# Performance work log

Hardware: AMD Instinct MI355X
Metric: run time of the kernel (lower is better)

The kernel has to match this reference:

```python
import jax, jax.numpy as jnp
import numpy as np

B, T, D = 8, 2048, 1024
S, W = 512, 16  # num spans, span width


def setup_inputs() -> dict:
    key = jax.random.key(0)
    k1, k2, k3, k4, k5, k6, k7 = jax.random.split(key, 7)
    text_tensor = jax.random.normal(k1, (B, T, D), dtype=jnp.float32)
    contextualized_embedding = jax.random.normal(k2, (B, T, D), dtype=jnp.float32)
    word_indices = jax.random.randint(k3, (B, S, W), 0, T, dtype=jnp.int64)
    word_mask = jax.random.randint(k4, (B, S, W), 0, 2, dtype=jnp.int64)
    word_indices_mask = jax.random.randint(k5, (B, S), 0, 2, dtype=jnp.int64)
    # Linear(input_dim, 1) params
    att_w = jax.random.normal(k6, (D, 1), dtype=jnp.float32) / np.sqrt(D)
    att_b = jax.random.normal(k7, (1,), dtype=jnp.float32) * 0.01
    return {
        "text_tensor": text_tensor,
        "contextualized_embedding": contextualized_embedding,
        "word_indices": word_indices,
        "word_mask": word_mask,
        "word_indices_mask": word_indices_mask,
        "att_w": att_w,
        "att_b": att_b,
    }


def reference(text_tensor, contextualized_embedding, word_indices, word_mask,
              word_indices_mask, att_w, att_b):
    b, t, d = text_tensor.shape
    s, w = word_indices.shape[1], word_indices.shape[2]
    # per-token attention logits: [B, T]
    global_logits = (jnp.einsum("btd,do->bto", text_tensor, att_w) + att_b)[..., 0]
    # relu on indices (clamp negatives to 0), then batched gather
    idx = jnp.maximum(word_indices, 0).astype(jnp.int32)  # [B, S, W]
    flat_idx = idx.reshape(b, s * w)
    # gather span embeddings: [B, S, W, D]
    span_emb = jnp.take_along_axis(text_tensor, flat_idx[:, :, None], axis=1)
    span_emb = span_emb.reshape(b, s, w, d)
    # gather span logits: [B, S, W]
    span_logits = jnp.take_along_axis(global_logits, flat_idx, axis=1).reshape(b, s, w)
    # masked softmax over span width
    mask = word_mask.astype(jnp.bool_)
    masked_logits = jnp.where(mask, span_logits, jnp.float32(-1e9))
    weights = jax.nn.softmax(masked_logits, axis=-1) * mask.astype(span_logits.dtype)
    # weighted sum pooling: [B, S, D]
    attended = jnp.einsum("bswd,bsw->bsd", span_emb, weights)
    return attended * word_indices_mask.astype(attended.dtype)[..., None]
```

## Files before the change

kernel.cpp:

```cpp
#include <hip/hip_runtime.h>

#define NB 8
#define NT 2048
#define ND 1024
#define NS 512
#define NW 16

typedef float f32x4 __attribute__((ext_vector_type(4)));

__global__ __launch_bounds__(64) void span_attn_kernel(
    const float* __restrict__ text,
    const int*   __restrict__ wi,
    const int*   __restrict__ wm,
    const int*   __restrict__ wim,
    const float* __restrict__ att_w,
    const float* __restrict__ att_b,
    float*       __restrict__ out)
{
    const int b    = blockIdx.x & (NB - 1);
    const int s    = blockIdx.x >> 3;
    const int bs   = b * NS + s;
    const int lane = threadIdx.x;

    float* orow = out + (size_t)bs * ND + 4 * lane;

    if (wim[bs] == 0) {
        #pragma unroll
        for (int k = 0; k < 4; ++k)
            __builtin_nontemporal_store((f32x4){0.f, 0.f, 0.f, 0.f},
                reinterpret_cast<f32x4*>(orow + 256 * k));
        return;
    }

    const int* wip = wi + (size_t)bs * NW;
    const int* wmp = wm + (size_t)bs * NW;

    unsigned mkbits = 0;
    #pragma unroll
    for (int q = 0; q < 4; ++q) {
        const int4 mv = *reinterpret_cast<const int4*>(wmp + 4 * q);
        mkbits |= (mv.x != 0 ? 1u : 0u) << (4 * q + 0);
        mkbits |= (mv.y != 0 ? 1u : 0u) << (4 * q + 1);
        mkbits |= (mv.z != 0 ? 1u : 0u) << (4 * q + 2);
        mkbits |= (mv.w != 0 ? 1u : 0u) << (4 * q + 3);
    }

    f32x4 wfrag[4];
    #pragma unroll
    for (int k = 0; k < 4; ++k)
        wfrag[k] = *reinterpret_cast<const f32x4*>(att_w + 4 * lane + 256 * k);
    const float bias = att_b[0];

    const float* tbase = text + (size_t)b * NT * ND + 4 * lane;

    f32x4 acc[4];
    #pragma unroll
    for (int k = 0; k < 4; ++k) acc[k] = (f32x4){0.f, 0.f, 0.f, 0.f};
    float esum = 0.0f;

    unsigned mask = mkbits;

    while (__popc(mask) >= 4) {
        const int r0 = __builtin_ctz(mask); mask &= mask - 1;
        const int r1 = __builtin_ctz(mask); mask &= mask - 1;
        const int r2 = __builtin_ctz(mask); mask &= mask - 1;
        const int r3 = __builtin_ctz(mask); mask &= mask - 1;
        const int i0 = wip[r0], i1 = wip[r1], i2 = wip[r2], i3 = wip[r3];
        const float* s0 = tbase + (size_t)(i0 > 0 ? i0 : 0) * ND;
        const float* s1 = tbase + (size_t)(i1 > 0 ? i1 : 0) * ND;
        const float* s2 = tbase + (size_t)(i2 > 0 ? i2 : 0) * ND;
        const float* s3 = tbase + (size_t)(i3 > 0 ? i3 : 0) * ND;
        f32x4 f0[4], f1[4], f2[4], f3[4];
        #pragma unroll
        for (int k = 0; k < 4; ++k) {
            f0[k] = *reinterpret_cast<const f32x4*>(s0 + 256 * k);
            f1[k] = *reinterpret_cast<const f32x4*>(s1 + 256 * k);
            f2[k] = *reinterpret_cast<const f32x4*>(s2 + 256 * k);
            f3[k] = *reinterpret_cast<const f32x4*>(s3 + 256 * k);
        }
        float d0 = 0.f, d1 = 0.f, d2 = 0.f, d3 = 0.f;
        #pragma unroll
        for (int k = 0; k < 4; ++k) {
            d0 += f0[k].x * wfrag[k].x + f0[k].y * wfrag[k].y
                + f0[k].z * wfrag[k].z + f0[k].w * wfrag[k].w;
            d1 += f1[k].x * wfrag[k].x + f1[k].y * wfrag[k].y
                + f1[k].z * wfrag[k].z + f1[k].w * wfrag[k].w;
            d2 += f2[k].x * wfrag[k].x + f2[k].y * wfrag[k].y
                + f2[k].z * wfrag[k].z + f2[k].w * wfrag[k].w;
            d3 += f3[k].x * wfrag[k].x + f3[k].y * wfrag[k].y
                + f3[k].z * wfrag[k].z + f3[k].w * wfrag[k].w;
        }
        #pragma unroll
        for (int sh = 1; sh < 64; sh <<= 1) {
            d0 += __shfl_xor(d0, sh);
            d1 += __shfl_xor(d1, sh);
            d2 += __shfl_xor(d2, sh);
            d3 += __shfl_xor(d3, sh);
        }
        const float e0 = __expf(d0 + bias);
        const float e1 = __expf(d1 + bias);
        const float e2 = __expf(d2 + bias);
        const float e3 = __expf(d3 + bias);
        esum += (e0 + e1) + (e2 + e3);
        #pragma unroll
        for (int k = 0; k < 4; ++k) {
            acc[k].x += e0 * f0[k].x + e1 * f1[k].x + e2 * f2[k].x + e3 * f3[k].x;
            acc[k].y += e0 * f0[k].y + e1 * f1[k].y + e2 * f2[k].y + e3 * f3[k].y;
            acc[k].z += e0 * f0[k].z + e1 * f1[k].z + e2 * f2[k].z + e3 * f3[k].z;
            acc[k].w += e0 * f0[k].w + e1 * f1[k].w + e2 * f2[k].w + e3 * f3[k].w;
        }
    }

    if (__popc(mask) >= 2) {
        const int r0 = __builtin_ctz(mask); mask &= mask - 1;
        const int r1 = __builtin_ctz(mask); mask &= mask - 1;
        const int i0 = wip[r0], i1 = wip[r1];
        const float* s0 = tbase + (size_t)(i0 > 0 ? i0 : 0) * ND;
        const float* s1 = tbase + (size_t)(i1 > 0 ? i1 : 0) * ND;
        f32x4 f0[4], f1[4];
        #pragma unroll
        for (int k = 0; k < 4; ++k) {
            f0[k] = *reinterpret_cast<const f32x4*>(s0 + 256 * k);
            f1[k] = *reinterpret_cast<const f32x4*>(s1 + 256 * k);
        }
        float d0 = 0.f, d1 = 0.f;
        #pragma unroll
        for (int k = 0; k < 4; ++k) {
            d0 += f0[k].x * wfrag[k].x + f0[k].y * wfrag[k].y
                + f0[k].z * wfrag[k].z + f0[k].w * wfrag[k].w;
            d1 += f1[k].x * wfrag[k].x + f1[k].y * wfrag[k].y
                + f1[k].z * wfrag[k].z + f1[k].w * wfrag[k].w;
        }
        #pragma unroll
        for (int sh = 1; sh < 64; sh <<= 1) {
            d0 += __shfl_xor(d0, sh);
            d1 += __shfl_xor(d1, sh);
        }
        const float e0 = __expf(d0 + bias);
        const float e1 = __expf(d1 + bias);
        esum += e0 + e1;
        #pragma unroll
        for (int k = 0; k < 4; ++k) {
            acc[k].x += e0 * f0[k].x + e1 * f1[k].x;
            acc[k].y += e0 * f0[k].y + e1 * f1[k].y;
            acc[k].z += e0 * f0[k].z + e1 * f1[k].z;
            acc[k].w += e0 * f0[k].w + e1 * f1[k].w;
        }
    }

    if (mask) {
        const int r0 = __builtin_ctz(mask);
        const int i0 = wip[r0];
        const float* s0 = tbase + (size_t)(i0 > 0 ? i0 : 0) * ND;
        f32x4 f0[4];
        #pragma unroll
        for (int k = 0; k < 4; ++k)
            f0[k] = *reinterpret_cast<const f32x4*>(s0 + 256 * k);
        float d0 = 0.f;
        #pragma unroll
        for (int k = 0; k < 4; ++k)
            d0 += f0[k].x * wfrag[k].x + f0[k].y * wfrag[k].y
                + f0[k].z * wfrag[k].z + f0[k].w * wfrag[k].w;
        #pragma unroll
        for (int sh = 1; sh < 64; sh <<= 1)
            d0 += __shfl_xor(d0, sh);
        const float e0 = __expf(d0 + bias);
        esum += e0;
        #pragma unroll
        for (int k = 0; k < 4; ++k) {
            acc[k].x += e0 * f0[k].x;
            acc[k].y += e0 * f0[k].y;
            acc[k].z += e0 * f0[k].z;
            acc[k].w += e0 * f0[k].w;
        }
    }

    const float inv = esum > 0.0f ? 1.0f / esum : 0.0f;
    #pragma unroll
    for (int k = 0; k < 4; ++k) {
        f32x4 o = acc[k];
        o.x *= inv; o.y *= inv; o.z *= inv; o.w *= inv;
        __builtin_nontemporal_store(o, reinterpret_cast<f32x4*>(orow + 256 * k));
    }
}

extern "C" void kernel_launch(void* const* d_in, const int* in_sizes, int n_in,
                              void* d_out, int out_size, void* d_ws, size_t ws_size,
                              hipStream_t stream) {
    const float* text  = (const float*)d_in[0];
    const int*   wi    = (const int*)d_in[2];
    const int*   wm    = (const int*)d_in[3];
    const int*   wim   = (const int*)d_in[4];
    const float* att_w = (const float*)d_in[5];
    const float* att_b = (const float*)d_in[6];
    float*       out   = (float*)d_out;

    span_attn_kernel<<<dim3(NB * NS), dim3(64), 0, stream>>>(
        text, wi, wm, wim, att_w, att_b, out);
}
```

Measured before the change: 15.48 us.

## Use persistent blocks with atomic work-stealing over spans per batch

The launch shrinks to 2048 blocks. Each block first handles one statically assigned span, then claims further spans from a per-batch atomic counter until all 512 spans in that batch are done. The aim is to balance the uneven per-span work that comes from the random masks, and to cut block launch overhead. In exchange it adds a memset launch, one atomic per span, and a serial dependency on the counter.

Result: slower. 26.72 us (+72.6%).

```diff
diff --git a/kernel.cpp b/kernel.cpp
--- a/kernel.cpp
+++ b/kernel.cpp
@@ -15,172 +15,180 @@
     const int*   __restrict__ wim,
     const float* __restrict__ att_w,
     const float* __restrict__ att_b,
-    float*       __restrict__ out)
+    float*       __restrict__ out,
+    unsigned*    __restrict__ counters)
 {
+    const int lane = threadIdx.x;
     const int b    = blockIdx.x & (NB - 1);
-    const int s    = blockIdx.x >> 3;
-    const int bs   = b * NS + s;
-    const int lane = threadIdx.x;
-
-    float* orow = out + (size_t)bs * ND + 4 * lane;
-
-    if (wim[bs] == 0) {
-        #pragma unroll
-        for (int k = 0; k < 4; ++k)
-            __builtin_nontemporal_store((f32x4){0.f, 0.f, 0.f, 0.f},
-                reinterpret_cast<f32x4*>(orow + 256 * k));
-        return;
-    }
-
-    const int* wip = wi + (size_t)bs * NW;
-    const int* wmp = wm + (size_t)bs * NW;
-
-    unsigned mkbits = 0;
-    #pragma unroll
-    for (int q = 0; q < 4; ++q) {
-        const int4 mv = *reinterpret_cast<const int4*>(wmp + 4 * q);
-        mkbits |= (mv.x != 0 ? 1u : 0u) << (4 * q + 0);
-        mkbits |= (mv.y != 0 ? 1u : 0u) << (4 * q + 1);
-        mkbits |= (mv.z != 0 ? 1u : 0u) << (4 * q + 2);
-        mkbits |= (mv.w != 0 ? 1u : 0u) << (4 * q + 3);
-    }
+    unsigned* ctr  = counters + b * 16;
 
     f32x4 wfrag[4];
     #pragma unroll
     for (int k = 0; k < 4; ++k)
         wfrag[k] = *reinterpret_cast<const f32x4*>(att_w + 4 * lane + 256 * k);
     const float bias = att_b[0];
-
     const float* tbase = text + (size_t)b * NT * ND + 4 * lane;
 
-    f32x4 acc[4];
-    #pragma unroll
-    for (int k = 0; k < 4; ++k) acc[k] = (f32x4){0.f, 0.f, 0.f, 0.f};
-    float esum = 0.0f;
-
-    unsigned mask = mkbits;
-
-    while (__popc(mask) >= 4) {
-        const int r0 = __builtin_ctz(mask); mask &= mask - 1;
-        const int r1 = __builtin_ctz(mask); mask &= mask - 1;
-        const int r2 = __builtin_ctz(mask); mask &= mask - 1;
-        const int r3 = __builtin_ctz(mask); mask &= mask - 1;
-        const int i0 = wip[r0], i1 = wip[r1], i2 = wip[r2], i3 = wip[r3];
-        const float* s0 = tbase + (size_t)(i0 > 0 ? i0 : 0) * ND;
-        const float* s1 = tbase + (size_t)(i1 > 0 ? i1 : 0) * ND;
-        const float* s2 = tbase + (size_t)(i2 > 0 ? i2 : 0) * ND;
-        const float* s3 = tbase + (size_t)(i3 > 0 ? i3 : 0) * ND;
-        f32x4 f0[4], f1[4], f2[4], f3[4];
-        #pragma unroll
-        for (int k = 0; k < 4; ++k) {
-            f0[k] = *reinterpret_cast<const f32x4*>(s0 + 256 * k);
-            f1[k] = *reinterpret_cast<const f32x4*>(s1 + 256 * k);
-            f2[k] = *reinterpret_cast<const f32x4*>(s2 + 256 * k);
-            f3[k] = *reinterpret_cast<const f32x4*>(s3 + 256 * k);
+    int s = blockIdx.x >> 3;
+
+    while (true) {
+        const int bs = b * NS + s;
+        float* orow = out + (size_t)bs * ND + 4 * lane;
+
+        if (wim[bs] == 0) {
+            #pragma unroll
+            for (int k = 0; k < 4; ++k)
+                __builtin_nontemporal_store((f32x4){0.f, 0.f, 0.f, 0.f},
+                    reinterpret_cast<f32x4*>(orow + 256 * k));
+        } else {
+            const int* wip = wi + (size_t)bs * NW;
+            const int* wmp = wm + (size_t)bs * NW;
+
+            unsigned mask = 0;
+            #pragma unroll
+            for (int q = 0; q < 4; ++q) {
+                const int4 mv = *reinterpret_cast<const int4*>(wmp + 4 * q);
+                mask |= (mv.x != 0 ? 1u : 0u) << (4 * q + 0);
+                mask |= (mv.y != 0 ? 1u : 0u) << (4 * q + 1);
+                mask |= (mv.z != 0 ? 1u : 0u) << (4 * q + 2);
+                mask |= (mv.w != 0 ? 1u : 0u) << (4 * q + 3);
+            }
+
+            f32x4 acc[4];
+            #pragma unroll
+            for (int k = 0; k < 4; ++k) acc[k] = (f32x4){0.f, 0.f, 0.f, 0.f};
+            float esum = 0.0f;
+
+            while (__popc(mask) >= 4) {
+                const int r0 = __builtin_ctz(mask); mask &= mask - 1;
+                const int r1 = __builtin_ctz(mask); mask &= mask - 1;
+                const int r2 = __builtin_ctz(mask); mask &= mask - 1;
+                const int r3 = __builtin_ctz(mask); mask &= mask - 1;
+                const int i0 = wip[r0], i1 = wip[r1], i2 = wip[r2], i3 = wip[r3];
+                const float* s0 = tbase + (size_t)(i0 > 0 ? i0 : 0) * ND;
+                const float* s1 = tbase + (size_t)(i1 > 0 ? i1 : 0) * ND;
+                const float* s2 = tbase + (size_t)(i2 > 0 ? i2 : 0) * ND;
+                const float* s3 = tbase + (size_t)(i3 > 0 ? i3 : 0) * ND;
+                f32x4 f0[4], f1[4], f2[4], f3[4];
+                #pragma unroll
+                for (int k = 0; k < 4; ++k) {
+                    f0[k] = *reinterpret_cast<const f32x4*>(s0 + 256 * k);
+                    f1[k] = *reinterpret_cast<const f32x4*>(s1 + 256 * k);
+                    f2[k] = *reinterpret_cast<const f32x4*>(s2 + 256 * k);
+                    f3[k] = *reinterpret_cast<const f32x4*>(s3 + 256 * k);
+                }
+                float d0 = 0.f, d1 = 0.f, d2 = 0.f, d3 = 0.f;
+                #pragma unroll
+                for (int k = 0; k < 4; ++k) {
+                    d0 += f0[k].x * wfrag[k].x + f0[k].y * wfrag[k].y
+                        + f0[k].z * wfrag[k].z + f0[k].w * wfrag[k].w;
+                    d1 += f1[k].x * wfrag[k].x + f1[k].y * wfrag[k].y
+                        + f1[k].z * wfrag[k].z + f1[k].w * wfrag[k].w;
+                    d2 += f2[k].x * wfrag[k].x + f2[k].y * wfrag[k].y
+                        + f2[k].z * wfrag[k].z + f2[k].w * wfrag[k].w;
+                    d3 += f3[k].x * wfrag[k].x + f3[k].y * wfrag[k].y
+                        + f3[k].z * wfrag[k].z + f3[k].w * wfrag[k].w;
+                }
+                #pragma unroll
+                for (int sh = 1; sh < 64; sh <<= 1) {
+                    d0 += __shfl_xor(d0, sh);
+                    d1 += __shfl_xor(d1, sh);
+                    d2 += __shfl_xor(d2, sh);
+                    d3 += __shfl_xor(d3, sh);
+                }
+                const float e0 = __expf(d0 + bias);
+                const float e1 = __expf(d1 + bias);
+                const float e2 = __expf(d2 + bias);
+                const float e3 = __expf(d3 + bias);
+                esum += (e0 + e1) + (e2 + e3);
+                #pragma unroll
+                for (int k = 0; k < 4; ++k) {
+                    acc[k].x += e0 * f0[k].x + e1 * f1[k].x + e2 * f2[k].x + e3 * f3[k].x;
+                    acc[k].y += e0 * f0[k].y + e1 * f1[k].y + e2 * f2[k].y + e3 * f3[k].y;
+                    acc[k].z += e0 * f0[k].z + e1 * f1[k].z + e2 * f2[k].z + e3 * f3[k].z;
+                    acc[k].w += e0 * f0[k].w + e1 * f1[k].w + e2 * f2[k].w + e3 * f3[k].w;
+                }
+            }
+
+            if (__popc(mask) >= 2) {
+                const int r0 = __builtin_ctz(mask); mask &= mask - 1;
+                const int r1 = __builtin_ctz(mask); mask &= mask - 1;
+                const int i0 = wip[r0], i1 = wip[r1];
+                const float* s0 = tbase + (size_t)(i0 > 0 ? i0 : 0) * ND;
+                const float* s1 = tbase + (size_t)(i1 > 0 ? i1 : 0) * ND;
+                f32x4 f0[4], f1[4];
+                #pragma unroll
+                for (int k = 0; k < 4; ++k) {
+                    f0[k] = *reinterpret_cast<const f32x4*>(s0 + 256 * k);
+                    f1[k] = *reinterpret_cast<const f32x4*>(s1 + 256 * k);
+                }
+                float d0 = 0.f, d1 = 0.f;
+                #pragma unroll
+                for (int k = 0; k < 4; ++k) {
+                    d0 += f0[k].x * wfrag[k].x + f0[k].y * wfrag[k].y
+                        + f0[k].z * wfrag[k].z + f0[k].w * wfrag[k].w;
+                    d1 += f1[k].x * wfrag[k].x + f1[k].y * wfrag[k].y
+                        + f1[k].z * wfrag[k].z + f1[k].w * wfrag[k].w;
+                }
+                #pragma unroll
+                for (int sh = 1; sh < 64; sh <<= 1) {
+                    d0 += __shfl_xor(d0, sh);
+                    d1 += __shfl_xor(d1, sh);
+                }
+                const float e0 = __expf(d0 + bias);
+                const float e1 = __expf(d1 + bias);
+                esum += e0 + e1;
+                #pragma unroll
+                for (int k = 0; k < 4; ++k) {
+                    acc[k].x += e0 * f0[k].x + e1 * f1[k].x;
+                    acc[k].y += e0 * f0[k].y + e1 * f1[k].y;
+                    acc[k].z += e0 * f0[k].z + e1 * f1[k].z;
+                    acc[k].w += e0 * f0[k].w + e1 * f1[k].w;
+                }
+            }
+
+            if (mask) {
+                const int r0 = __builtin_ctz(mask);
+                const int i0 = wip[r0];
+                const float* s0 = tbase + (size_t)(i0 > 0 ? i0 : 0) * ND;
+                f32x4 f0[4];
+                #pragma unroll
+                for (int k = 0; k < 4; ++k)
+                    f0[k] = *reinterpret_cast<const f32x4*>(s0 + 256 * k);
+                float d0 = 0.f;
+                #pragma unroll
+                for (int k = 0; k < 4; ++k)
+                    d0 += f0[k].x * wfrag[k].x + f0[k].y * wfrag[k].y
+                        + f0[k].z * wfrag[k].z + f0[k].w * wfrag[k].w;
+                #pragma unroll
+                for (int sh = 1; sh < 64; sh <<= 1)
+                    d0 += __shfl_xor(d0, sh);
+                const float e0 = __expf(d0 + bias);
+                esum += e0;
+                #pragma unroll
+                for (int k = 0; k < 4; ++k) {
+                    acc[k].x += e0 * f0[k].x;
+                    acc[k].y += e0 * f0[k].y;
+                    acc[k].z += e0 * f0[k].z;
+                    acc[k].w += e0 * f0[k].w;
+                }
+            }
+
+            const float inv = esum > 0.0f ? 1.0f / esum : 0.0f;
+            #pragma unroll
+            for (int k = 0; k < 4; ++k) {
+                f32x4 o = acc[k];
+                o.x *= inv; o.y *= inv; o.z *= inv; o.w *= inv;
+                __builtin_nontemporal_store(o,
+                    reinterpret_cast<f32x4*>(orow + 256 * k));
+            }
         }
-        float d0 = 0.f, d1 = 0.f, d2 = 0.f, d3 = 0.f;
-        #pragma unroll
-        for (int k = 0; k < 4; ++k) {
-            d0 += f0[k].x * wfrag[k].x + f0[k].y * wfrag[k].y
-                + f0[k].z * wfrag[k].z + f0[k].w * wfrag[k].w;
-            d1 += f1[k].x * wfrag[k].x + f1[k].y * wfrag[k].y
-                + f1[k].z * wfrag[k].z + f1[k].w * wfrag[k].w;
-            d2 += f2[k].x * wfrag[k].x + f2[k].y * wfrag[k].y
-                + f2[k].z * wfrag[k].z + f2[k].w * wfrag[k].w;
-            d3 += f3[k].x * wfrag[k].x + f3[k].y * wfrag[k].y
-                + f3[k].z * wfrag[k].z + f3[k].w * wfrag[k].w;
-        }
-        #pragma unroll
-        for (int sh = 1; sh < 64; sh <<= 1) {
-            d0 += __shfl_xor(d0, sh);
-            d1 += __shfl_xor(d1, sh);
-            d2 += __shfl_xor(d2, sh);
-            d3 += __shfl_xor(d3, sh);
-        }
-        const float e0 = __expf(d0 + bias);
-        const float e1 = __expf(d1 + bias);
-        const float e2 = __expf(d2 + bias);
-        const float e3 = __expf(d3 + bias);
-        esum += (e0 + e1) + (e2 + e3);
-        #pragma unroll
-        for (int k = 0; k < 4; ++k) {
-            acc[k].x += e0 * f0[k].x + e1 * f1[k].x + e2 * f2[k].x + e3 * f3[k].x;
-            acc[k].y += e0 * f0[k].y + e1 * f1[k].y + e2 * f2[k].y + e3 * f3[k].y;
-            acc[k].z += e0 * f0[k].z + e1 * f1[k].z + e2 * f2[k].z + e3 * f3[k].z;
-            acc[k].w += e0 * f0[k].w + e1 * f1[k].w + e2 * f2[k].w + e3 * f3[k].w;
-        }
-    }
-
-    if (__popc(mask) >= 2) {
-        const int r0 = __builtin_ctz(mask); mask &= mask - 1;
-        const int r1 = __builtin_ctz(mask); mask &= mask - 1;
-        const int i0 = wip[r0], i1 = wip[r1];
-        const float* s0 = tbase + (size_t)(i0 > 0 ? i0 : 0) * ND;
-        const float* s1 = tbase + (size_t)(i1 > 0 ? i1 : 0) * ND;
-        f32x4 f0[4], f1[4];
-        #pragma unroll
-        for (int k = 0; k < 4; ++k) {
-            f0[k] = *reinterpret_cast<const f32x4*>(s0 + 256 * k);
-            f1[k] = *reinterpret_cast<const f32x4*>(s1 + 256 * k);
-        }
-        float d0 = 0.f, d1 = 0.f;
-        #pragma unroll
-        for (int k = 0; k < 4; ++k) {
-            d0 += f0[k].x * wfrag[k].x + f0[k].y * wfrag[k].y
-                + f0[k].z * wfrag[k].z + f0[k].w * wfrag[k].w;
-            d1 += f1[k].x * wfrag[k].x + f1[k].y * wfrag[k].y
-                + f1[k].z * wfrag[k].z + f1[k].w * wfrag[k].w;
-        }
-        #pragma unroll
-        for (int sh = 1; sh < 64; sh <<= 1) {
-            d0 += __shfl_xor(d0, sh);
-            d1 += __shfl_xor(d1, sh);
-        }
-        const float e0 = __expf(d0 + bias);
-        const float e1 = __expf(d1 + bias);
-        esum += e0 + e1;
-        #pragma unroll
-        for (int k = 0; k < 4; ++k) {
-            acc[k].x += e0 * f0[k].x + e1 * f1[k].x;
-            acc[k].y += e0 * f0[k].y + e1 * f1[k].y;
-            acc[k].z += e0 * f0[k].z + e1 * f1[k].z;
-            acc[k].w += e0 * f0[k].w + e1 * f1[k].w;
-        }
-    }
-
-    if (mask) {
-        const int r0 = __builtin_ctz(mask);
-        const int i0 = wip[r0];
-        const float* s0 = tbase + (size_t)(i0 > 0 ? i0 : 0) * ND;
-        f32x4 f0[4];
-        #pragma unroll
-        for (int k = 0; k < 4; ++k)
-            f0[k] = *reinterpret_cast<const f32x4*>(s0 + 256 * k);
-        float d0 = 0.f;
-        #pragma unroll
-        for (int k = 0; k < 4; ++k)
-            d0 += f0[k].x * wfrag[k].x + f0[k].y * wfrag[k].y
-                + f0[k].z * wfrag[k].z + f0[k].w * wfrag[k].w;
-        #pragma unroll
-        for (int sh = 1; sh < 64; sh <<= 1)
-            d0 += __shfl_xor(d0, sh);
-        const float e0 = __expf(d0 + bias);
-        esum += e0;
-        #pragma unroll
-        for (int k = 0; k < 4; ++k) {
-            acc[k].x += e0 * f0[k].x;
-            acc[k].y += e0 * f0[k].y;
-            acc[k].z += e0 * f0[k].z;
-            acc[k].w += e0 * f0[k].w;
-        }
-    }
-
-    const float inv = esum > 0.0f ? 1.0f / esum : 0.0f;
-    #pragma unroll
-    for (int k = 0; k < 4; ++k) {
-        f32x4 o = acc[k];
-        o.x *= inv; o.y *= inv; o.z *= inv; o.w *= inv;
-        __builtin_nontemporal_store(o, reinterpret_cast<f32x4*>(orow + 256 * k));
+
+        unsigned n = 0;
+        if (lane == 0) n = atomicAdd(ctr, 1u);
+        n = (unsigned)__shfl((int)n, 0);
+        if (n >= (unsigned)(NS - 256)) break;
+        s = 256 + (int)n;
     }
 }
 
@@ -194,7 +202,9 @@
     const float* att_w = (const float*)d_in[5];
     const float* att_b = (const float*)d_in[6];
     float*       out   = (float*)d_out;
-
-    span_attn_kernel<<<dim3(NB * NS), dim3(64), 0, stream>>>(
-        text, wi, wm, wim, att_w, att_b, out);
+    unsigned*    ctrs  = (unsigned*)d_ws;
+
+    hipMemsetAsync(d_ws, 0, 8 * 16 * sizeof(unsigned), stream);
+    span_attn_kernel<<<dim3(2048), dim3(64), 0, stream>>>(
+        text, wi, wm, wim, att_w, att_b, out, ctrs);
 }
```
